# Performance work log

Hardware: AMD Instinct MI355X
Metric: run time of the kernel (lower is better)

The kernel has to match this reference:

```python
import math
import jax, jax.numpy as jnp
import numpy as np

HIDDEN = 1024
HEADS = 16
HEAD = HIDDEN // HEADS
BUCKET = 32
MAXPOS = 512
REL = 2 * BUCKET - 1
EPS = 1e-7
L, B = 512, 16
STD = math.sqrt(2.0 / (5.0 * HIDDEN))


def _ln(x, g=None, b=None):
    m = x.mean(-1, keepdims=True)
    v = ((x - m) ** 2).mean(-1, keepdims=True)
    y = (x - m) * jax.lax.rsqrt(v + EPS)
    return y if g is None else y * g + b


def _bucket_indices(n):
    # DeBERTa-style log bucket relative positions, shifted to [0, 2*BUCKET-2]
    r = jnp.arange(n)[:, None] - jnp.arange(n)[None, :]
    mid = BUCKET // 2
    abs_pos = jnp.where((r < mid) & (r > -mid), mid - 1,
                        jnp.clip(jnp.abs(r), None, MAXPOS - 1))
    log_pos = jnp.ceil(jnp.log(abs_pos.astype(jnp.float32) / mid)
                       / math.log((MAXPOS - 1) / mid) * (mid - 1)).astype(jnp.int32) + mid
    bucket_pos = jnp.where(abs_pos <= mid, r, log_pos * jnp.sign(r))
    return (BUCKET - 1 + bucket_pos).astype(jnp.int32)


def setup_inputs() -> dict:
    key = jax.random.key(0)
    ks = jax.random.split(key, 8)
    return {
        'hidden_states': jax.random.normal(ks[0], (L, B, HIDDEN), jnp.float32),
        'attention_mask': jax.random.randint(ks[1], (B, 1, 1, L), 0, 2).astype(bool),
        'relative_embedding': jax.random.normal(ks[2], (REL, HIDDEN), jnp.float32),
        'wqk': jax.random.normal(ks[3], (2 * HIDDEN, HIDDEN), jnp.float32) * STD,
        'bqk': jnp.zeros((2 * HIDDEN,), jnp.float32),
        'wv': jax.random.normal(ks[4], (HIDDEN, HIDDEN), jnp.float32) * STD,
        'bv': jnp.zeros((HIDDEN,), jnp.float32),
        'wo': jax.random.normal(ks[5], (HIDDEN, HIDDEN), jnp.float32) * STD,
        'bo': jnp.zeros((HIDDEN,), jnp.float32),
        'ln_g': jnp.ones((HIDDEN,), jnp.float32),
        'ln_b': jnp.zeros((HIDDEN,), jnp.float32),
    }


def reference(hidden_states, attention_mask, relative_embedding,
              wqk, bqk, wv, bv, wo, bo, ln_g, ln_b):
    Lq, Bq, D = hidden_states.shape
    scale = 1.0 / math.sqrt(3 * HEAD)
    h = _ln(hidden_states)                                 # pre LN, no affine
    q, k = jnp.split(h @ wqk.T + bqk, 2, axis=-1)
    v = h @ wv.T + bv
    qpos, kpos = jnp.split(relative_embedding @ wqk.T + bqk, 2, axis=-1)
    qpos = qpos.reshape(REL, HEADS, HEAD)
    kpos = kpos.reshape(REL, HEADS, HEAD)
    # (L,B,D) -> (B,H,L,hd)
    qh = q.reshape(Lq, Bq, HEADS, HEAD).transpose(1, 2, 0, 3)
    kh = k.reshape(Lq, Bq, HEADS, HEAD).transpose(1, 2, 0, 3)
    vh = v.reshape(Lq, Bq, HEADS, HEAD).transpose(1, 2, 0, 3)
    scores = jnp.einsum('bhqd,bhkd->bhqk', qh, kh) * scale       # c2c
    qp = jnp.einsum('bhqd,khd->bhqk', qh, kpos) * scale          # c2p (k over buckets)
    pk = jnp.einsum('bhkd,qhd->bhqk', kh, qpos) * scale          # p2c (q over buckets)
    idx = jnp.broadcast_to(_bucket_indices(Lq), (Bq, HEADS, Lq, Lq))
    scores = scores + jnp.take_along_axis(qp, idx, axis=-1) \
                    + jnp.take_along_axis(pk, idx, axis=-2)
    # masked softmax: mask==True -> -inf before softmax, 0 after
    probs = jax.nn.softmax(jnp.where(attention_mask, -1e9, scores), axis=-1)
    probs = jnp.where(attention_mask, 0.0, probs)
    ctx = jnp.einsum('bhqk,bhkd->bhqd', probs, vh)
    ctx = ctx.transpose(2, 0, 1, 3).reshape(Lq, Bq, D)           # (L,B,D)
    out = ctx @ wo.T + bo
    return _ln(out, ln_g, ln_b)
```

## Files before the change

### kernel.cpp

```cpp
#include <hip/hip_runtime.h>
#include <hip/hip_bf16.h>

#define HID 1024
#define HEADS 16
#define HEAD 64
#define RELN 63
#define SEQ 512
#define BATCH 16
#define NROWS (SEQ*BATCH)
#define MEXT 8320
#define NQKV 3072
#define LNEPS 1e-7f
#define SCALE2 (0.07216878364870323f * 1.4426950408889634f)

typedef __attribute__((ext_vector_type(4))) float  f32x4;
typedef __attribute__((ext_vector_type(8))) short  s16x8;
typedef __attribute__((ext_vector_type(4))) ushort u16x4;

static __device__ __forceinline__ ushort f2bf(float f) {
  union { float f; unsigned u; } v; v.f = f;
  unsigned r = v.u + 0x7fffu + ((v.u >> 16) & 1u);
  return (ushort)(r >> 16);
}
static __device__ __forceinline__ float bf2f(ushort u) {
  union { unsigned u; float f; } v; v.u = ((unsigned)u) << 16;
  return v.f;
}

__global__ void k_prep(const void* mask_raw, const float* bqk, const float* bv,
                       ushort* mask01, int* idx_tab, float* bcat) {
  __shared__ int s_isbool;
  int tid = threadIdx.x;
  if (tid == 0) s_isbool = 0;
  __syncthreads();
  const unsigned* mu = (const unsigned*)mask_raw;
  int bad = 0;
  for (int i = tid; i < 2048; i += 256) if (mu[i] > 1u) bad = 1;
  if (bad) s_isbool = 1;
  __syncthreads();
  int isbool = s_isbool;
  const unsigned char* m8 = (const unsigned char*)mask_raw;
  const int* m32 = (const int*)mask_raw;
  for (int i = tid; i < BATCH*SEQ; i += 256) {
    int m = isbool ? (int)m8[i] : m32[i];
    mask01[i] = m ? 1 : 0;
  }
  for (int i = tid; i < 1023; i += 256) {
    int r = i - 511;
    int a = r < 0 ? -r : r;
    int absp = (a < 16) ? 15 : (a < 511 ? a : 511);
    int idx;
    if (absp <= 16) idx = 31 + r;
    else {
      float v = logf((float)absp / 16.0f) / logf(511.0f / 16.0f) * 15.0f;
      int lp = (int)ceilf(v) + 16;
      idx = 31 + (r > 0 ? lp : -lp);
    }
    idx_tab[i] = idx;
  }
  for (int i = tid; i < 2048; i += 256) bcat[i] = bqk[i];
  for (int i = tid; i < 1024; i += 256) bcat[2048 + i] = bv[i];
}

__global__ __launch_bounds__(256) void k_convert(const float* wqk, const float* wv, const float* wo,
                                                 ushort* wcat, ushort* wo_b) {
  int c = blockIdx.x * 256 + threadIdx.x;
  f32x4 x; ushort* dst;
  if (c < 524288)      { x = *(const f32x4*)(wqk + (size_t)c * 4);            dst = wcat + (size_t)c * 4; }
  else if (c < 786432) { x = *(const f32x4*)(wv  + (size_t)(c - 524288) * 4); dst = wcat + (size_t)c * 4; }
  else                 { x = *(const f32x4*)(wo  + (size_t)(c - 786432) * 4); dst = wo_b + (size_t)(c - 786432) * 4; }
  u16x4 o = { f2bf(x[0]), f2bf(x[1]), f2bf(x[2]), f2bf(x[3]) };
  *(u16x4*)dst = o;
}

__global__ __launch_bounds__(256) void k_ln1(const float* hid, const float* rel, ushort* h_ext) {
  int row = blockIdx.x, tid = threadIdx.x;
  __shared__ float red[8];
  if (row < NROWS) {
    const float* src = hid + (size_t)row * HID;
    f32x4 x = *(const f32x4*)(src + tid * 4);
    float s = x[0] + x[1] + x[2] + x[3];
    #pragma unroll
    for (int m = 1; m < 64; m <<= 1) s += __shfl_xor(s, m);
    if ((tid & 63) == 0) red[tid >> 6] = s;
    __syncthreads();
    float mean = (red[0] + red[1] + red[2] + red[3]) * (1.0f / HID);
    float d0 = x[0] - mean, d1 = x[1] - mean, d2 = x[2] - mean, d3 = x[3] - mean;
    float sq = d0*d0 + d1*d1 + d2*d2 + d3*d3;
    #pragma unroll
    for (int m = 1; m < 64; m <<= 1) sq += __shfl_xor(sq, m);
    __syncthreads();
    if ((tid & 63) == 0) red[4 + (tid >> 6)] = sq;
    __syncthreads();
    float var = (red[4] + red[5] + red[6] + red[7]) * (1.0f / HID);
    float rs = rsqrtf(var + LNEPS);
    u16x4 o = { f2bf(d0*rs), f2bf(d1*rs), f2bf(d2*rs), f2bf(d3*rs) };
    *(u16x4*)(h_ext + (size_t)row * HID + tid * 4) = o;
  } else if (row < NROWS + RELN) {
    const float* src = rel + (size_t)(row - NROWS) * HID;
    f32x4 x = *(const f32x4*)(src + tid * 4);
    u16x4 o = { f2bf(x[0]), f2bf(x[1]), f2bf(x[2]), f2bf(x[3]) };
    *(u16x4*)(h_ext + (size_t)row * HID + tid * 4) = o;
  } else {
    u16x4 z = { 0, 0, 0, 0 };
    *(u16x4*)(h_ext + (size_t)row * HID + tid * 4) = z;
  }
}

template<int WRITE_F32>
__global__ __launch_bounds__(256) void k_gemm(const ushort* A, const ushort* Bw, const float* bias,
                                              ushort* Cb, float* Cf, int M, int N, int K) {
  __shared__ char smem[32768];
  char* As = smem;
  char* Bs = smem + 16384;
  int tid = threadIdx.x, lane = tid & 63, w = tid >> 6;
  int nbn = N >> 7;
  int per = gridDim.x >> 3;
  int gl = (blockIdx.x & 7) * per + (blockIdx.x >> 3);
  int bm = gl / nbn, bn = gl % nbn;
  int wr = w >> 1, wc = w & 1;
  int g = lane >> 4, r = lane & 15;
  f32x4 acc[4][4] = {};
  for (int ko = 0; ko < K; ko += 64) {
    __syncthreads();
    #pragma unroll
    for (int c = 0; c < 4; ++c) {
      int chunk = c * 256 + tid;
      int row = chunk >> 3;
      int kb = (chunk & 7) << 4;
      int kbs = kb ^ ((row & 7) << 4);
      const char* gA = (const char*)(A + (size_t)(bm * 128 + row) * K + ko) + kbs;
      const char* gB = (const char*)(Bw + (size_t)(bn * 128 + row) * K + ko) + kbs;
      __builtin_amdgcn_global_load_lds((const __attribute__((address_space(1))) void*)gA,
                                       (__attribute__((address_space(3))) void*)(As + c * 4096 + w * 1024),
                                       16, 0, 0);
      __builtin_amdgcn_global_load_lds((const __attribute__((address_space(1))) void*)gB,
                                       (__attribute__((address_space(3))) void*)(Bs + c * 4096 + w * 1024),
                                       16, 0, 0);
    }
    __syncthreads();
    #pragma unroll
    for (int kk = 0; kk < 2; ++kk) {
      s16x8 af[4], bf[4];
      #pragma unroll
      for (int mt = 0; mt < 4; ++mt) {
        int row = wr * 64 + mt * 16 + r;
        int kb = (kk * 64 + g * 16) ^ ((row & 7) << 4);
        af[mt] = *(const s16x8*)(As + row * 128 + kb);
      }
      #pragma unroll
      for (int nt = 0; nt < 4; ++nt) {
        int row = wc * 64 + nt * 16 + r;
        int kb = (kk * 64 + g * 16) ^ ((row & 7) << 4);
        bf[nt] = *(const s16x8*)(Bs + row * 128 + kb);
      }
      #pragma unroll
      for (int mt = 0; mt < 4; ++mt)
        #pragma unroll
        for (int nt = 0; nt < 4; ++nt)
          acc[mt][nt] = __builtin_amdgcn_mfma_f32_16x16x32_bf16(af[mt], bf[nt], acc[mt][nt], 0, 0, 0);
    }
  }
  #pragma unroll
  for (int nt = 0; nt < 4; ++nt) {
    int col = bn * 128 + wc * 64 + nt * 16 + r;
    float bvv = bias[col];
    #pragma unroll
    for (int mt = 0; mt < 4; ++mt) {
      int row0 = bm * 128 + wr * 64 + mt * 16 + g * 4;
      #pragma unroll
      for (int i = 0; i < 4; ++i) {
        float v = acc[mt][nt][i] + bvv;
        if (WRITE_F32) Cf[(size_t)(row0 + i) * N + col] = v;
        else           Cb[(size_t)(row0 + i) * N + col] = f2bf(v);
      }
    }
  }
}

__global__ __launch_bounds__(256) void k_pos(const ushort* qkv, const ushort* mask01,
                                             ushort* qp, ushort* pk) {
  int bh = blockIdx.x;
  int b = bh >> 4, h = bh & 15;
  int tid = threadIdx.x, lane = tid & 63, w = tid >> 6;
  int g = lane >> 4, r = lane & 15;
  __shared__ ushort mb[512];
  for (int i = tid; i < 512; i += 256) mb[i] = mask01[b * SEQ + i];
  __syncthreads();
  s16x8 bkp[4][2], bqp[4][2];
  #pragma unroll
  for (int nt = 0; nt < 4; ++nt)
    #pragma unroll
    for (int kk = 0; kk < 2; ++kk) {
      size_t rowp = (size_t)(NROWS + nt * 16 + r);
      int colq = h * 64 + kk * 32 + g * 8;
      bqp[nt][kk] = *(const s16x8*)(qkv + rowp * NQKV + colq);
      bkp[nt][kk] = *(const s16x8*)(qkv + rowp * NQKV + 1024 + colq);
    }
  for (int cc = 0; cc < 8; ++cc) {
    int rowbase = cc * 64 + w * 16;
    s16x8 aq[2], ak[2];
    #pragma unroll
    for (int kk = 0; kk < 2; ++kk) {
      size_t rowq = (size_t)((rowbase + r) * 16 + b);
      int colq = h * 64 + kk * 32 + g * 8;
      aq[kk] = *(const s16x8*)(qkv + rowq * NQKV + colq);
      ak[kk] = *(const s16x8*)(qkv + rowq * NQKV + 1024 + colq);
    }
    f32x4 accq[4] = {}, acck[4] = {};
    #pragma unroll
    for (int kk = 0; kk < 2; ++kk)
      #pragma unroll
      for (int nt = 0; nt < 4; ++nt) {
        accq[nt] = __builtin_amdgcn_mfma_f32_16x16x32_bf16(aq[kk], bkp[nt][kk], accq[nt], 0, 0, 0);
        acck[nt] = __builtin_amdgcn_mfma_f32_16x16x32_bf16(ak[kk], bqp[nt][kk], acck[nt], 0, 0, 0);
      }
    #pragma unroll
    for (int nt = 0; nt < 4; ++nt)
      #pragma unroll
      for (int i = 0; i < 4; ++i) {
        int q = rowbase + g * 4 + i;
        int t = nt * 16 + r;
        float biasv = mb[q] ? -1e9f : 0.0f;
        qp[(size_t)bh * SEQ * 64 + q * 64 + t] = f2bf(accq[nt][i] * SCALE2);
        pk[(size_t)bh * SEQ * 64 + q * 64 + t] = f2bf(acck[nt][i] * SCALE2 + biasv);
      }
  }
}

__global__ __launch_bounds__(256) void k_vt(const ushort* qkv, ushort* vt, ushort* kc) {
  int bid = blockIdx.x;
  int bh = bid >> 3, lt = bid & 7;
  int b = bh >> 4, h = bh & 15;
  __shared__ ushort tile[64][72];
  int tid = threadIdx.x;
  #pragma unroll
  for (int c = 0; c < 2; ++c) {
    int e = (c * 256 + tid) * 8;
    int l = e >> 6, d0 = e & 63;
    size_t row = (size_t)((lt * 64 + l) * 16 + b);
    s16x8 kv = *(const s16x8*)(qkv + row * NQKV + 1024 + h * 64 + d0);
    #pragma unroll
    for (int j = 0; j < 8; ++j) kv[j] = (short)f2bf(bf2f((ushort)kv[j]) * SCALE2);
    *(s16x8*)(kc + ((size_t)bh * SEQ + lt * 64 + l) * 64 + d0) = kv;
    *(s16x8*)&tile[l][d0] = *(const s16x8*)(qkv + row * NQKV + 2048 + h * 64 + d0);
  }
  __syncthreads();
  #pragma unroll
  for (int c = 0; c < 2; ++c) {
    int e = (c * 256 + tid) * 8;
    int d = e >> 6, l0 = e & 63;
    ushort tmp[8];
    #pragma unroll
    for (int j = 0; j < 8; ++j) tmp[j] = tile[l0 + j][d];
    *(s16x8*)(vt + (size_t)(bh * 64 + d) * SEQ + lt * 64 + l0) = *(s16x8*)tmp;
  }
}

__global__ __launch_bounds__(512) void k_attn(const ushort* qkv, const ushort* qp_all, const ushort* pk_all,
                                              const ushort* kc, const ushort* vt,
                                              const int* idx_tab, ushort* ctx) {
  int bid = blockIdx.x;
  int slot = bid >> 3;
  int bh = (bid & 7) * 32 + (slot >> 2);
  int qt0 = (slot & 3) * 2;
  int b = bh >> 4, h = bh & 15;
  int tid = threadIdx.x, lane = tid & 63, w = tid >> 6;
  int g = lane >> 4, r = lane & 15;
  int qsub = w >> 2, wq = w & 3;

  __shared__ char   Ks[8192];
  __shared__ ushort qp_s[128][68];
  __shared__ ushort pk_s[64][68];
  __shared__ ushort p_s[8][16][68];
  __shared__ ushort idx_s[1024];

  const size_t qp_base = (size_t)bh * SEQ * 64 + (size_t)qt0 * 4096;
  const size_t pk_base = (size_t)bh * SEQ * 64;
  const char* kcb = (const char*)(kc + (size_t)bh * SEQ * 64);

  int krow = tid >> 3;
  int ksrccol = ((tid & 7) ^ (krow & 7)) << 4;
  int prow = tid >> 3, pcol8 = (tid & 7) * 8;

  {
    const char* src = kcb + (size_t)krow * 128 + ksrccol;
    __builtin_amdgcn_global_load_lds((const __attribute__((address_space(1))) void*)src,
                                     (__attribute__((address_space(3))) void*)(Ks + w * 1024),
                                     16, 0, 0);
  }
  s16x8 pkreg = *(const s16x8*)(pk_all + pk_base + (size_t)tid * 8);
  #pragma unroll
  for (int c = 0; c < 4; ++c) {
    int chunk = c * 512 + tid;
    int row = chunk >> 4, col4 = (chunk & 15) * 4;
    *(u16x4*)&qp_s[row][col4] = *(const u16x4*)(qp_all + qp_base + (size_t)row * 64 + col4);
  }
  for (int i = tid; i < 1023; i += 512) idx_s[i] = (ushort)idx_tab[i];
  s16x8 aq[2];
  int qg0 = (qt0 + qsub) * 64 + wq * 16;
  #pragma unroll
  for (int kk = 0; kk < 2; ++kk) {
    size_t row = (size_t)((qg0 + r) * 16 + b);
    aq[kk] = *(const s16x8*)(qkv + row * NQKV + h * 64 + kk * 32 + g * 8);
  }
  {
    u16x4 lo = { (ushort)pkreg[0], (ushort)pkreg[1], (ushort)pkreg[2], (ushort)pkreg[3] };
    u16x4 hi = { (ushort)pkreg[4], (ushort)pkreg[5], (ushort)pkreg[6], (ushort)pkreg[7] };
    *(u16x4*)&pk_s[prow][pcol8] = lo;
    *(u16x4*)&pk_s[prow][pcol8 + 4] = hi;
  }
  __syncthreads();

  float m_i = -3e38f, l_i = 0.0f;
  f32x4 o_acc[4] = {};
  const ushort* qprow = &qp_s[qsub * 64 + wq * 16 + r][0];
  const int qglob511 = (qt0 + qsub) * 64 + wq * 16 + r + 511;

  for (int kt = 0; kt < 8; ++kt) {
    if (kt < 7)
      pkreg = *(const s16x8*)(pk_all + pk_base + (size_t)(kt + 1) * 4096 + (size_t)tid * 8);

    f32x4 s[4];
    #pragma unroll
    for (int nt = 0; nt < 4; ++nt) {
      f32x4 a = {};
      #pragma unroll
      for (int kk = 0; kk < 2; ++kk) {
        s16x8 bk = *(const s16x8*)(Ks + (nt * 16 + r) * 128 + ((kk * 64 + g * 16) ^ ((r & 7) << 4)));
        a = __builtin_amdgcn_mfma_f32_16x16x32_bf16(bk, aq[kk], a, 0, 0, 0);
      }
      s[nt] = a;
    }

    float m_loc = -3e38f;
    #pragma unroll
    for (int nt = 0; nt < 4; ++nt) {
      #pragma unroll
      for (int i = 0; i < 4; ++i) {
        int kl = nt * 16 + g * 4 + i;
        int t = idx_s[qglob511 - kt * 64 - kl];
        float v = s[nt][i] + bf2f(qprow[t]) + bf2f(pk_s[kl][t]);
        s[nt][i] = v;
        m_loc = fmaxf(m_loc, v);
      }
    }
    __syncthreads();

    if (kt < 7) {
      const char* src = kcb + (size_t)(kt + 1) * 8192 + (size_t)krow * 128 + ksrccol;
      __builtin_amdgcn_global_load_lds((const __attribute__((address_space(1))) void*)src,
                                       (__attribute__((address_space(3))) void*)(Ks + w * 1024),
                                       16, 0, 0);
      u16x4 lo = { (ushort)pkreg[0], (ushort)pkreg[1], (ushort)pkreg[2], (ushort)pkreg[3] };
      u16x4 hi = { (ushort)pkreg[4], (ushort)pkreg[5], (ushort)pkreg[6], (ushort)pkreg[7] };
      *(u16x4*)&pk_s[prow][pcol8] = lo;
      *(u16x4*)&pk_s[prow][pcol8 + 4] = hi;
    }
    s16x8 vreg[2][4];
    #pragma unroll
    for (int kk = 0; kk < 2; ++kk)
      #pragma unroll
      for (int nt = 0; nt < 4; ++nt)
        vreg[kk][nt] = *(const s16x8*)(vt + (size_t)(bh * 64 + nt * 16 + r) * SEQ + kt * 64 + kk * 32 + g * 8);

    float mx = fmaxf(m_loc, __shfl_xor(m_loc, 16));
    mx = fmaxf(mx, __shfl_xor(mx, 32));

    if (__any(mx > m_i + 8.0f)) {
      float mnew = fmaxf(m_i, mx);
      float rs = exp2f(m_i - mnew);
      m_i = mnew;
      l_i *= rs;
      float rsb[4];
      #pragma unroll
      for (int i = 0; i < 4; ++i) rsb[i] = __shfl(rs, g * 4 + i);
      #pragma unroll
      for (int nt = 0; nt < 4; ++nt)
        #pragma unroll
        for (int i = 0; i < 4; ++i) o_acc[nt][i] *= rsb[i];
    }

    float psum = 0.0f;
    #pragma unroll
    for (int nt = 0; nt < 4; ++nt) {
      u16x4 pk4;
      #pragma unroll
      for (int i = 0; i < 4; ++i) {
        float pe = exp2f(s[nt][i] - m_i);
        psum += pe;
        pk4[i] = f2bf(pe);
      }
      *(u16x4*)&p_s[w][r][nt * 16 + g * 4] = pk4;
    }
    psum += __shfl_xor(psum, 16);
    psum += __shfl_xor(psum, 32);
    l_i += psum;

    #pragma unroll
    for (int kk = 0; kk < 2; ++kk) {
      u16x4 lo = *(const u16x4*)&p_s[w][r][kk * 32 + g * 8];
      u16x4 hi = *(const u16x4*)&p_s[w][r][kk * 32 + g * 8 + 4];
      s16x8 pa = { (short)lo[0], (short)lo[1], (short)lo[2], (short)lo[3],
                   (short)hi[0], (short)hi[1], (short)hi[2], (short)hi[3] };
      #pragma unroll
      for (int nt = 0; nt < 4; ++nt)
        o_acc[nt] = __builtin_amdgcn_mfma_f32_16x16x32_bf16(pa, vreg[kk][nt], o_acc[nt], 0, 0, 0);
    }

    if (kt < 7) __syncthreads();
  }

  float lb[4];
  #pragma unroll
  for (int i = 0; i < 4; ++i) lb[i] = __shfl(l_i, g * 4 + i);
  #pragma unroll
  for (int i = 0; i < 4; ++i) {
    float inv = lb[i] > 0.0f ? 1.0f / lb[i] : 0.0f;
    int lq = (qt0 + qsub) * 64 + wq * 16 + g * 4 + i;
    size_t rowc = (size_t)(lq * 16 + b);
    #pragma unroll
    for (int nt = 0; nt < 4; ++nt)
      ctx[rowc * HID + h * 64 + nt * 16 + r] = f2bf(o_acc[nt][i] * inv);
  }
}

__global__ __launch_bounds__(256) void k_ln2(const ushort* tmpb, const float* gamma, const float* beta,
                                             float* out) {
  int row = blockIdx.x, tid = threadIdx.x;
  __shared__ float red[8];
  u16x4 xb = *(const u16x4*)(tmpb + (size_t)row * HID + tid * 4);
  float x[4] = { bf2f(xb[0]), bf2f(xb[1]), bf2f(xb[2]), bf2f(xb[3]) };
  float s = x[0] + x[1] + x[2] + x[3];
  #pragma unroll
  for (int m = 1; m < 64; m <<= 1) s += __shfl_xor(s, m);
  if ((tid & 63) == 0) red[tid >> 6] = s;
  __syncthreads();
  float mean = (red[0] + red[1] + red[2] + red[3]) * (1.0f / HID);
  float d[4]; float sq = 0.0f;
  #pragma unroll
  for (int j = 0; j < 4; ++j) { d[j] = x[j] - mean; sq += d[j] * d[j]; }
  #pragma unroll
  for (int m = 1; m < 64; m <<= 1) sq += __shfl_xor(sq, m);
  __syncthreads();
  if ((tid & 63) == 0) red[4 + (tid >> 6)] = sq;
  __syncthreads();
  float var = (red[4] + red[5] + red[6] + red[7]) * (1.0f / HID);
  float rs = rsqrtf(var + LNEPS);
  f32x4 o;
  #pragma unroll
  for (int j = 0; j < 4; ++j) o[j] = d[j] * rs * gamma[tid * 4 + j] + beta[tid * 4 + j];
  *(f32x4*)(out + (size_t)row * HID + tid * 4) = o;
}

extern "C" void kernel_launch(void* const* d_in, const int* in_sizes, int n_in,
                              void* d_out, int out_size, void* d_ws, size_t ws_size,
                              hipStream_t stream) {
  (void)in_sizes; (void)n_in; (void)out_size; (void)ws_size;
  const float* hid  = (const float*)d_in[0];
  const void*  mask = d_in[1];
  const float* rel  = (const float*)d_in[2];
  const float* wqk  = (const float*)d_in[3];
  const float* bqk  = (const float*)d_in[4];
  const float* wv   = (const float*)d_in[5];
  const float* bv   = (const float*)d_in[6];
  const float* wo   = (const float*)d_in[7];
  const float* bo   = (const float*)d_in[8];
  const float* ln_g = (const float*)d_in[9];
  const float* ln_b = (const float*)d_in[10];

  char* ws = (char*)d_ws;
  ushort* wcat     = (ushort*)(ws);
  ushort* wo_b     = (ushort*)(ws + 6291456);
  float*  bcat     = (float*) (ws + 8388608);
  ushort* mask01   = (ushort*)(ws + 8400896);
  int*    idx_tab  = (int*)   (ws + 8433664);
  ushort* h_ext    = (ushort*)(ws + 8437760);
  ushort* qkv      = (ushort*)(ws + 25477120);
  ushort* qp_b     = (ushort*)(ws + 76595200);
  ushort* pk_b     = (ushort*)(ws + 93372416);
  ushort* vt       = (ushort*)(ws + 110149632);
  char*   tmpr     = (ws + 126926848);
  ushort* ctx = h_ext;
  ushort* kc   = (ushort*)tmpr;
  ushort* tmpb = (ushort*)tmpr;

  k_prep<<<1, 256, 0, stream>>>(mask, bqk, bv, mask01, idx_tab, bcat);
  k_convert<<<4096, 256, 0, stream>>>(wqk, wv, wo, wcat, wo_b);
  k_ln1<<<MEXT, 256, 0, stream>>>(hid, rel, h_ext);
  k_gemm<0><<<(MEXT / 128) * (NQKV / 128), 256, 0, stream>>>(h_ext, wcat, bcat, qkv, nullptr, MEXT, NQKV, 1024);
  k_pos<<<256, 256, 0, stream>>>(qkv, mask01, qp_b, pk_b);
  k_vt<<<2048, 256, 0, stream>>>(qkv, vt, kc);
  k_attn<<<1024, 512, 0, stream>>>(qkv, qp_b, pk_b, kc, vt, idx_tab, ctx);
  k_gemm<0><<<(NROWS / 128) * (1024 / 128), 256, 0, stream>>>(ctx, wo_b, bo, tmpb, nullptr, NROWS, 1024, 1024);
  k_ln2<<<NROWS, 256, 0, stream>>>(tmpb, ln_g, ln_b, (float*)d_out);
}
```

Before: 265.3 us.

## Process 256 queries per attention block with K/V fragments loaded straight from global

The attention kernel now covers 256 queries per block instead of 128, launching half as many blocks. Each wave handles two 16-query sub-tiles, so every K and V fragment it loads serves both. The per-tile K staging in LDS through global_load_lds, the pk prefetch and the in-loop barriers are removed. The full 512-row pk table and a 256-row qp table are loaded into shared memory up front, and K fragments are read directly from global memory. This cuts barrier and staging overhead, but it raises LDS use sharply (about 110 KB), which lowers occupancy, and it relies on caches for the unswizzled K reads.

```diff
diff --git a/kernel.cpp b/kernel.cpp
--- a/kernel.cpp
+++ b/kernel.cpp
@@ -262,166 +262,155 @@
                                               const int* idx_tab, ushort* ctx) {
   int bid = blockIdx.x;
   int slot = bid >> 3;
-  int bh = (bid & 7) * 32 + (slot >> 2);
-  int qt0 = (slot & 3) * 2;
+  int bh = (bid & 7) * 32 + (slot >> 1);
+  int qh = slot & 1;
   int b = bh >> 4, h = bh & 15;
   int tid = threadIdx.x, lane = tid & 63, w = tid >> 6;
   int g = lane >> 4, r = lane & 15;
-  int qsub = w >> 2, wq = w & 3;
-
-  __shared__ char   Ks[8192];
-  __shared__ ushort qp_s[128][68];
-  __shared__ ushort pk_s[64][68];
+
+  __shared__ ushort pk_f[512][68];
+  __shared__ ushort qp_s[256][68];
   __shared__ ushort p_s[8][16][68];
   __shared__ ushort idx_s[1024];
 
-  const size_t qp_base = (size_t)bh * SEQ * 64 + (size_t)qt0 * 4096;
-  const size_t pk_base = (size_t)bh * SEQ * 64;
-  const char* kcb = (const char*)(kc + (size_t)bh * SEQ * 64);
-
-  int krow = tid >> 3;
-  int ksrccol = ((tid & 7) ^ (krow & 7)) << 4;
-  int prow = tid >> 3, pcol8 = (tid & 7) * 8;
-
-  {
-    const char* src = kcb + (size_t)krow * 128 + ksrccol;
-    __builtin_amdgcn_global_load_lds((const __attribute__((address_space(1))) void*)src,
-                                     (__attribute__((address_space(3))) void*)(Ks + w * 1024),
-                                     16, 0, 0);
-  }
-  s16x8 pkreg = *(const s16x8*)(pk_all + pk_base + (size_t)tid * 8);
+  const ushort* qpsrc = qp_all + (size_t)bh * SEQ * 64 + (size_t)qh * 256 * 64;
+  const ushort* pksrc = pk_all + (size_t)bh * SEQ * 64;
+  const char*   kcb   = (const char*)(kc + (size_t)bh * SEQ * 64);
+
   #pragma unroll
   for (int c = 0; c < 4; ++c) {
     int chunk = c * 512 + tid;
-    int row = chunk >> 4, col4 = (chunk & 15) * 4;
-    *(u16x4*)&qp_s[row][col4] = *(const u16x4*)(qp_all + qp_base + (size_t)row * 64 + col4);
+    int row = chunk >> 3, col8 = (chunk & 7) * 8;
+    s16x8 v = *(const s16x8*)(qpsrc + (size_t)row * 64 + col8);
+    u16x4 lo = { (ushort)v[0], (ushort)v[1], (ushort)v[2], (ushort)v[3] };
+    u16x4 hi = { (ushort)v[4], (ushort)v[5], (ushort)v[6], (ushort)v[7] };
+    *(u16x4*)&qp_s[row][col8] = lo;
+    *(u16x4*)&qp_s[row][col8 + 4] = hi;
+  }
+  #pragma unroll
+  for (int c = 0; c < 8; ++c) {
+    int chunk = c * 512 + tid;
+    int row = chunk >> 3, col8 = (chunk & 7) * 8;
+    s16x8 v = *(const s16x8*)(pksrc + (size_t)row * 64 + col8);
+    u16x4 lo = { (ushort)v[0], (ushort)v[1], (ushort)v[2], (ushort)v[3] };
+    u16x4 hi = { (ushort)v[4], (ushort)v[5], (ushort)v[6], (ushort)v[7] };
+    *(u16x4*)&pk_f[row][col8] = lo;
+    *(u16x4*)&pk_f[row][col8 + 4] = hi;
   }
   for (int i = tid; i < 1023; i += 512) idx_s[i] = (ushort)idx_tab[i];
-  s16x8 aq[2];
-  int qg0 = (qt0 + qsub) * 64 + wq * 16;
-  #pragma unroll
-  for (int kk = 0; kk < 2; ++kk) {
-    size_t row = (size_t)((qg0 + r) * 16 + b);
-    aq[kk] = *(const s16x8*)(qkv + row * NQKV + h * 64 + kk * 32 + g * 8);
-  }
-  {
-    u16x4 lo = { (ushort)pkreg[0], (ushort)pkreg[1], (ushort)pkreg[2], (ushort)pkreg[3] };
-    u16x4 hi = { (ushort)pkreg[4], (ushort)pkreg[5], (ushort)pkreg[6], (ushort)pkreg[7] };
-    *(u16x4*)&pk_s[prow][pcol8] = lo;
-    *(u16x4*)&pk_s[prow][pcol8 + 4] = hi;
-  }
-  __syncthreads();
-
-  float m_i = -3e38f, l_i = 0.0f;
-  f32x4 o_acc[4] = {};
-  const ushort* qprow = &qp_s[qsub * 64 + wq * 16 + r][0];
-  const int qglob511 = (qt0 + qsub) * 64 + wq * 16 + r + 511;
+  s16x8 aq[2][2];
+  #pragma unroll
+  for (int qs = 0; qs < 2; ++qs)
+    #pragma unroll
+    for (int kk = 0; kk < 2; ++kk) {
+      int qglob = qh * 256 + qs * 128 + w * 16 + r;
+      aq[qs][kk] = *(const s16x8*)(qkv + ((size_t)qglob * 16 + b) * NQKV + h * 64 + kk * 32 + g * 8);
+    }
+  __syncthreads();
+
+  float m_i[2] = { -3e38f, -3e38f }, l_i[2] = { 0.0f, 0.0f };
+  f32x4 o_acc[2][4] = {};
 
   for (int kt = 0; kt < 8; ++kt) {
-    if (kt < 7)
-      pkreg = *(const s16x8*)(pk_all + pk_base + (size_t)(kt + 1) * 4096 + (size_t)tid * 8);
-
-    f32x4 s[4];
-    #pragma unroll
-    for (int nt = 0; nt < 4; ++nt) {
-      f32x4 a = {};
+    s16x8 kf[4][2], vf[2][4];
+    #pragma unroll
+    for (int nt = 0; nt < 4; ++nt)
+      #pragma unroll
+      for (int kk = 0; kk < 2; ++kk)
+        kf[nt][kk] = *(const s16x8*)(kcb + (size_t)(kt * 64 + nt * 16 + r) * 128 + kk * 64 + g * 16);
+    #pragma unroll
+    for (int kk = 0; kk < 2; ++kk)
+      #pragma unroll
+      for (int nt = 0; nt < 4; ++nt)
+        vf[kk][nt] = *(const s16x8*)(vt + (size_t)(bh * 64 + nt * 16 + r) * SEQ + kt * 64 + kk * 32 + g * 8);
+
+    #pragma unroll
+    for (int qs = 0; qs < 2; ++qs) {
+      f32x4 s[4];
+      #pragma unroll
+      for (int nt = 0; nt < 4; ++nt) {
+        f32x4 a = {};
+        #pragma unroll
+        for (int kk = 0; kk < 2; ++kk)
+          a = __builtin_amdgcn_mfma_f32_16x16x32_bf16(kf[nt][kk], aq[qs][kk], a, 0, 0, 0);
+        s[nt] = a;
+      }
+
+      const ushort* qprow = &qp_s[qs * 128 + w * 16 + r][0];
+      const int qg511 = qh * 256 + qs * 128 + w * 16 + r + 511;
+      float m_loc = -3e38f;
+      #pragma unroll
+      for (int nt = 0; nt < 4; ++nt) {
+        #pragma unroll
+        for (int i = 0; i < 4; ++i) {
+          int kg = kt * 64 + nt * 16 + g * 4 + i;
+          int t = idx_s[qg511 - kg];
+          float v = s[nt][i] + bf2f(qprow[t]) + bf2f(pk_f[kg][t]);
+          s[nt][i] = v;
+          m_loc = fmaxf(m_loc, v);
+        }
+      }
+
+      float mx = fmaxf(m_loc, __shfl_xor(m_loc, 16));
+      mx = fmaxf(mx, __shfl_xor(mx, 32));
+
+      if (__any(mx > m_i[qs] + 8.0f)) {
+        float mnew = fmaxf(m_i[qs], mx);
+        float rs = exp2f(m_i[qs] - mnew);
+        m_i[qs] = mnew;
+        l_i[qs] *= rs;
+        float rsb[4];
+        #pragma unroll
+        for (int i = 0; i < 4; ++i) rsb[i] = __shfl(rs, g * 4 + i);
+        #pragma unroll
+        for (int nt = 0; nt < 4; ++nt)
+          #pragma unroll
+          for (int i = 0; i < 4; ++i) o_acc[qs][nt][i] *= rsb[i];
+      }
+
+      float psum = 0.0f;
+      #pragma unroll
+      for (int nt = 0; nt < 4; ++nt) {
+        u16x4 pk4;
+        #pragma unroll
+        for (int i = 0; i < 4; ++i) {
+          float pe = exp2f(s[nt][i] - m_i[qs]);
+          psum += pe;
+          pk4[i] = f2bf(pe);
+        }
+        *(u16x4*)&p_s[w][r][nt * 16 + g * 4] = pk4;
+      }
+      psum += __shfl_xor(psum, 16);
+      psum += __shfl_xor(psum, 32);
+      l_i[qs] += psum;
+
       #pragma unroll
       for (int kk = 0; kk < 2; ++kk) {
-        s16x8 bk = *(const s16x8*)(Ks + (nt * 16 + r) * 128 + ((kk * 64 + g * 16) ^ ((r & 7) << 4)));
-        a = __builtin_amdgcn_mfma_f32_16x16x32_bf16(bk, aq[kk], a, 0, 0, 0);
-      }
-      s[nt] = a;
-    }
-
-    float m_loc = -3e38f;
-    #pragma unroll
-    for (int nt = 0; nt < 4; ++nt) {
-      #pragma unroll
-      for (int i = 0; i < 4; ++i) {
-        int kl = nt * 16 + g * 4 + i;
-        int t = idx_s[qglob511 - kt * 64 - kl];
-        float v = s[nt][i] + bf2f(qprow[t]) + bf2f(pk_s[kl][t]);
-        s[nt][i] = v;
-        m_loc = fmaxf(m_loc, v);
-      }
-    }
-    __syncthreads();
-
-    if (kt < 7) {
-      const char* src = kcb + (size_t)(kt + 1) * 8192 + (size_t)krow * 128 + ksrccol;
-      __builtin_amdgcn_global_load_lds((const __attribute__((address_space(1))) void*)src,
-                                       (__attribute__((address_space(3))) void*)(Ks + w * 1024),
-                                       16, 0, 0);
-      u16x4 lo = { (ushort)pkreg[0], (ushort)pkreg[1], (ushort)pkreg[2], (ushort)pkreg[3] };
-      u16x4 hi = { (ushort)pkreg[4], (ushort)pkreg[5], (ushort)pkreg[6], (ushort)pkreg[7] };
-      *(u16x4*)&pk_s[prow][pcol8] = lo;
-      *(u16x4*)&pk_s[prow][pcol8 + 4] = hi;
-    }
-    s16x8 vreg[2][4];
-    #pragma unroll
-    for (int kk = 0; kk < 2; ++kk)
+        u16x4 lo = *(const u16x4*)&p_s[w][r][kk * 32 + g * 8];
+        u16x4 hi = *(const u16x4*)&p_s[w][r][kk * 32 + g * 8 + 4];
+        s16x8 pa = { (short)lo[0], (short)lo[1], (short)lo[2], (short)lo[3],
+                     (short)hi[0], (short)hi[1], (short)hi[2], (short)hi[3] };
+        #pragma unroll
+        for (int nt = 0; nt < 4; ++nt)
+          o_acc[qs][nt] = __builtin_amdgcn_mfma_f32_16x16x32_bf16(pa, vf[kk][nt], o_acc[qs][nt], 0, 0, 0);
+      }
+    }
+  }
+
+  #pragma unroll
+  for (int qs = 0; qs < 2; ++qs) {
+    float lb[4];
+    #pragma unroll
+    for (int i = 0; i < 4; ++i) lb[i] = __shfl(l_i[qs], g * 4 + i);
+    #pragma unroll
+    for (int i = 0; i < 4; ++i) {
+      float inv = lb[i] > 0.0f ? 1.0f / lb[i] : 0.0f;
+      int lq = qh * 256 + qs * 128 + w * 16 + g * 4 + i;
+      size_t rowc = (size_t)(lq * 16 + b);
       #pragma unroll
       for (int nt = 0; nt < 4; ++nt)
-        vreg[kk][nt] = *(const s16x8*)(vt + (size_t)(bh * 64 + nt * 16 + r) * SEQ + kt * 64 + kk * 32 + g * 8);
-
-    float mx = fmaxf(m_loc, __shfl_xor(m_loc, 16));
-    mx = fmaxf(mx, __shfl_xor(mx, 32));
-
-    if (__any(mx > m_i + 8.0f)) {
-      float mnew = fmaxf(m_i, mx);
-      float rs = exp2f(m_i - mnew);
-      m_i = mnew;
-      l_i *= rs;
-      float rsb[4];
-      #pragma unroll
-      for (int i = 0; i < 4; ++i) rsb[i] = __shfl(rs, g * 4 + i);
-      #pragma unroll
-      for (int nt = 0; nt < 4; ++nt)
-        #pragma unroll
-        for (int i = 0; i < 4; ++i) o_acc[nt][i] *= rsb[i];
-    }
-
-    float psum = 0.0f;
-    #pragma unroll
-    for (int nt = 0; nt < 4; ++nt) {
-      u16x4 pk4;
-      #pragma unroll
-      for (int i = 0; i < 4; ++i) {
-        float pe = exp2f(s[nt][i] - m_i);
-        psum += pe;
-        pk4[i] = f2bf(pe);
-      }
-      *(u16x4*)&p_s[w][r][nt * 16 + g * 4] = pk4;
-    }
-    psum += __shfl_xor(psum, 16);
-    psum += __shfl_xor(psum, 32);
-    l_i += psum;
-
-    #pragma unroll
-    for (int kk = 0; kk < 2; ++kk) {
-      u16x4 lo = *(const u16x4*)&p_s[w][r][kk * 32 + g * 8];
-      u16x4 hi = *(const u16x4*)&p_s[w][r][kk * 32 + g * 8 + 4];
-      s16x8 pa = { (short)lo[0], (short)lo[1], (short)lo[2], (short)lo[3],
-                   (short)hi[0], (short)hi[1], (short)hi[2], (short)hi[3] };
-      #pragma unroll
-      for (int nt = 0; nt < 4; ++nt)
-        o_acc[nt] = __builtin_amdgcn_mfma_f32_16x16x32_bf16(pa, vreg[kk][nt], o_acc[nt], 0, 0, 0);
-    }
-
-    if (kt < 7) __syncthreads();
-  }
-
-  float lb[4];
-  #pragma unroll
-  for (int i = 0; i < 4; ++i) lb[i] = __shfl(l_i, g * 4 + i);
-  #pragma unroll
-  for (int i = 0; i < 4; ++i) {
-    float inv = lb[i] > 0.0f ? 1.0f / lb[i] : 0.0f;
-    int lq = (qt0 + qsub) * 64 + wq * 16 + g * 4 + i;
-    size_t rowc = (size_t)(lq * 16 + b);
-    #pragma unroll
-    for (int nt = 0; nt < 4; ++nt)
-      ctx[rowc * HID + h * 64 + nt * 16 + r] = f2bf(o_acc[nt][i] * inv);
+        ctx[rowc * HID + h * 64 + nt * 16 + r] = f2bf(o_acc[qs][nt][i] * inv);
+    }
   }
 }
 
@@ -491,7 +480,7 @@
   k_gemm<0><<<(MEXT / 128) * (NQKV / 128), 256, 0, stream>>>(h_ext, wcat, bcat, qkv, nullptr, MEXT, NQKV, 1024);
   k_pos<<<256, 256, 0, stream>>>(qkv, mask01, qp_b, pk_b);
   k_vt<<<2048, 256, 0, stream>>>(qkv, vt, kc);
-  k_attn<<<1024, 512, 0, stream>>>(qkv, qp_b, pk_b, kc, vt, idx_tab, ctx);
+  k_attn<<<512, 512, 0, stream>>>(qkv, qp_b, pk_b, kc, vt, idx_tab, ctx);
   k_gemm<0><<<(NROWS / 128) * (1024 / 128), 256, 0, stream>>>(ctx, wo_b, bo, tmpb, nullptr, NROWS, 1024, 1024);
   k_ln2<<<NROWS, 256, 0, stream>>>(tmpb, ln_g, ln_b, (float*)d_out);
 }
```

New measurement: 255.6 us. 1.04x faster.
